# Kernel optimization log

Hardware: AMD Instinct MI355X
Metric: run time of the kernel (lower is better)

The kernel has to match this reference:

```python
import jax, jax.numpy as jnp
import numpy as np

IN_CH = 8        # input_channels (includes time channel)
HID = 64         # hidden_channels
OUT = 1          # output_channels
MLP_W = 128      # CDEFunc hidden width
B, T = 4096, 166


def setup_inputs() -> dict:
    key = jax.random.key(0)
    ks = jax.random.split(key, 12)
    s = lambda fan_in: 1.0 / np.sqrt(fan_in)
    u0 = jax.random.normal(ks[0], (B, IN_CH - 1), dtype=jnp.float32)
    coeffs = jax.random.normal(ks[1], (B, T, IN_CH), dtype=jnp.float32)
    # CDEFunc params
    W1 = jax.random.uniform(ks[2], (HID, MLP_W), jnp.float32, -s(HID), s(HID))
    b1 = jax.random.uniform(ks[3], (MLP_W,), jnp.float32, -s(HID), s(HID))
    W2 = jax.random.uniform(ks[4], (MLP_W, IN_CH * HID), jnp.float32, -s(MLP_W), s(MLP_W))
    b2 = jax.random.uniform(ks[5], (IN_CH * HID,), jnp.float32, -s(MLP_W), s(MLP_W))
    # initial / readout linears
    Wi = jax.random.uniform(ks[6], (IN_CH - 1, HID), jnp.float32, -s(IN_CH - 1), s(IN_CH - 1))
    bi = jax.random.uniform(ks[7], (HID,), jnp.float32, -s(IN_CH - 1), s(IN_CH - 1))
    Wr = jax.random.uniform(ks[8], (HID, OUT), jnp.float32, -s(HID), s(HID))
    br = jax.random.uniform(ks[9], (OUT,), jnp.float32, -s(HID), s(HID))
    return {"u0": u0, "coeffs": coeffs, "W1": W1, "b1": b1, "W2": W2,
            "b2": b2, "Wi": Wi, "bi": bi, "Wr": Wr, "br": br}


def _cde_forward(u0, coeffs, W1, b1, W2, b2, Wi, bi, Wr, br):
    z0 = u0 @ Wi + bi                                  # [B, HID]
    # Linear interpolation on the knot grid t=0..T-1 with Euler steps of dt=1:
    # z_{k+1} = z_k + f(z_k) @ (X_{k+1} - X_k)
    dX = coeffs[:, 1:] - coeffs[:, :-1]                # [B, T-1, IN_CH]
    dX_t = jnp.swapaxes(dX, 0, 1)                      # [T-1, B, IN_CH]

    def step(z, dx):
        h = jax.nn.relu(z @ W1 + b1)                   # [B, MLP_W]
        f = jnp.tanh(h @ W2 + b2)                      # [B, IN_CH*HID]
        f = f.reshape(z.shape[0], HID, IN_CH)          # [B, HID, IN_CH]
        z_new = z + jnp.einsum('bhi,bi->bh', f, dx)
        return z_new, z_new

    _, zs = jax.lax.scan(step, z0, dX_t)               # [T-1, B, HID]
    z_all = jnp.concatenate([z0[None], zs], axis=0)    # [T, B, HID]
    z_all = jnp.swapaxes(z_all, 0, 1)                  # [B, T, HID]
    return z_all @ Wr + br                             # [B, T, OUT]


def reference(u0, coeffs, W1, b1, W2, b2, Wi, bi, Wr, br):
    return _cde_forward(u0, coeffs, W1, b1, W2, b2, Wi, bi, Wr, br)
```

## Files before the change

### kernel.cpp

```cpp
#include <hip/hip_runtime.h>


#define NBLK 256
#define NT   512
#define RB   16
#define T_LEN 166
#define NSTEP 165
#define IC   8
#define HID  64
#define MW   128
#define NF   512

typedef _Float16 half8 __attribute__((ext_vector_type(8)));
typedef _Float16 half4 __attribute__((ext_vector_type(4)));
typedef float    f32x4 __attribute__((ext_vector_type(4)));

__device__ __forceinline__ float fast_tanh(float x) {
    float e = __expf(2.0f * x);
    return 1.0f - 2.0f * __builtin_amdgcn_rcpf(e + 1.0f);
}

__device__ __forceinline__ void bar_lgkm() {
    asm volatile("s_waitcnt lgkmcnt(0)" ::: "memory");
    __builtin_amdgcn_s_barrier();
    __builtin_amdgcn_sched_barrier(0);
}

__device__ __forceinline__ float sum_xor16(float x) {
#if __has_builtin(__builtin_amdgcn_permlane16_swap)
    auto r = __builtin_amdgcn_permlane16_swap(__float_as_uint(x), __float_as_uint(x), false, false);
    return __uint_as_float(r[0]) + __uint_as_float(r[1]);
#else
    return x + __shfl_xor(x, 16, 64);
#endif
}
__device__ __forceinline__ float sum_xor32(float x) {
#if __has_builtin(__builtin_amdgcn_permlane32_swap)
    auto r = __builtin_amdgcn_permlane32_swap(__float_as_uint(x), __float_as_uint(x), false, false);
    return __uint_as_float(r[0]) + __uint_as_float(r[1]);
#else
    return x + __shfl_xor(x, 32, 64);
#endif
}

__global__ __launch_bounds__(NT, 2)
void cde_fused(const float* __restrict__ u0, const float* __restrict__ coeffs,
               const float* __restrict__ W1, const float* __restrict__ b1,
               const float* __restrict__ W2, const float* __restrict__ b2,
               const float* __restrict__ Wi, const float* __restrict__ bi,
               const float* __restrict__ Wr, const float* __restrict__ br,
               float* __restrict__ out)
{
    __shared__ __align__(16) unsigned char hh[RB * 256];
    __shared__ __align__(16) unsigned char hl[RB * 256];
    __shared__ __align__(16) unsigned char zh[RB * 128];
    __shared__ __align__(16) unsigned char zl[RB * 128];
    __shared__ float part[8][17];

    const int tid  = threadIdx.x;
    const int lane = tid & 63;
    const int w    = tid >> 6;
    const int l15  = lane & 15;
    const int lq   = lane >> 4;
    const bool hi32 = (lane & 32) != 0;
    const int swzr = (l15 & 7) << 4;
    const int b0   = blockIdx.x * RB;

    half8 w1h[2], w1l[2];
    #pragma unroll
    for (int kt = 0; kt < 2; ++kt) {
        const int krow = kt * 32 + lq * 8;
        const int ncol = w * 16 + l15;
        half8 vh, vl;
        #pragma unroll
        for (int j = 0; j < 8; ++j) {
            const float x = W1[(krow + j) * MW + ncol];
            const _Float16 hi = (_Float16)x;
            vh[j] = hi; vl[j] = (_Float16)(x - (float)hi);
        }
        w1h[kt] = vh; w1l[kt] = vl;
    }
    half8 w2h[16], w2l[16];
    #pragma unroll
    for (int q = 0; q < 4; ++q) {
        #pragma unroll
        for (int kt = 0; kt < 4; ++kt) {
            const int krow = kt * 32 + lq * 8;
            const int ncol = (w * 4 + q) * 16 + l15;
            half8 vh, vl;
            #pragma unroll
            for (int j = 0; j < 8; ++j) {
                const float x = W2[(krow + j) * NF + ncol];
                const _Float16 hi = (_Float16)x;
                vh[j] = hi; vl[j] = (_Float16)(x - (float)hi);
            }
            w2h[q * 4 + kt] = vh; w2l[q * 4 + kt] = vl;
        }
    }
    const f32x4 b1v = *(const f32x4*)(b1 + w * 16 + lq * 4);
    f32x4 b2v[4];
    #pragma unroll
    for (int q = 0; q < 4; ++q)
        b2v[q] = *(const f32x4*)(b2 + (w * 4 + q) * 16 + lq * 4);

    float wrs[8];
    #pragma unroll
    for (int j = 0; j < 8; ++j) wrs[j] = Wr[w * 8 + j];
    const float brv = br[0];

    float z8[8];
    {
        float uu[7];
        const float* ur = u0 + (size_t)(b0 + l15) * 7;
        #pragma unroll
        for (int c = 0; c < 7; ++c) uu[c] = ur[c];
        #pragma unroll
        for (int j = 0; j < 8; ++j) {
            float a = bi[w * 8 + j];
            #pragma unroll
            for (int c = 0; c < 7; ++c) a = fmaf(uu[c], Wi[c * HID + w * 8 + j], a);
            z8[j] = a;
        }
    }
    {
        half8 hi8, lo8;
        float rp = 0.f;
        #pragma unroll
        for (int j = 0; j < 8; ++j) {
            const _Float16 hi = (_Float16)z8[j];
            hi8[j] = hi; lo8[j] = (_Float16)(z8[j] - (float)hi);
            rp = fmaf(z8[j], wrs[j], rp);
        }
        if (lq == 0) {
            const int zoff = l15 * 128 + ((w * 16) ^ swzr);
            *(half8*)(zh + zoff) = hi8;
            *(half8*)(zl + zoff) = lo8;
            part[w][l15] = rp;
        }
    }
    const float* cbase = coeffs + (size_t)(b0 + l15) * T_LEN * IC + (lq & 1) * 4;
    f32x4 ccur = *(const f32x4*)(cbase);
    __syncthreads();

    for (int t = 0; t < NSTEP; ++t) {
        const f32x4 cnext = *(const f32x4*)(cbase + (size_t)(t + 1) * IC);

        if (w == 7) {
            float v = part[lq][l15] + part[lq + 4][l15];
            v = sum_xor32(sum_xor16(v));
            if (lq == 0) out[(size_t)(b0 + l15) * T_LEN + t] = v + brv;
        }

        const int zo0 = l15 * 128 + ((lq * 16) ^ swzr);
        const int zo1 = l15 * 128 + ((64 + lq * 16) ^ swzr);
        const half8 zfh0 = *(const half8*)(zh + zo0);
        const half8 zfl0 = *(const half8*)(zl + zo0);
        const half8 zfh1 = *(const half8*)(zh + zo1);
        const half8 zfl1 = *(const half8*)(zl + zo1);
        f32x4 a1A = b1v;
        f32x4 a1B = {0.f, 0.f, 0.f, 0.f};
        a1A = __builtin_amdgcn_mfma_f32_16x16x32_f16(w1h[0], zfh0, a1A, 0, 0, 0);
        a1B = __builtin_amdgcn_mfma_f32_16x16x32_f16(w1h[1], zfh1, a1B, 0, 0, 0);
        a1A = __builtin_amdgcn_mfma_f32_16x16x32_f16(w1l[0], zfh0, a1A, 0, 0, 0);
        a1B = __builtin_amdgcn_mfma_f32_16x16x32_f16(w1l[1], zfh1, a1B, 0, 0, 0);
        a1A = __builtin_amdgcn_mfma_f32_16x16x32_f16(w1h[0], zfl0, a1A, 0, 0, 0);
        a1B = __builtin_amdgcn_mfma_f32_16x16x32_f16(w1h[1], zfl1, a1B, 0, 0, 0);
        half4 ph, pl;
        #pragma unroll
        for (int r = 0; r < 4; ++r) {
            const float hv = fmaxf(a1A[r] + a1B[r], 0.0f);
            const _Float16 hi = (_Float16)hv;
            ph[r] = hi; pl[r] = (_Float16)(hv - (float)hi);
        }
        const int hoff = l15 * 256 + ((w * 32 + lq * 8) ^ swzr);
        *(half4*)(hh + hoff) = ph;
        *(half4*)(hl + hoff) = pl;
        bar_lgkm();

        half8 bhf[4], blf[4];
        #pragma unroll
        for (int kt = 0; kt < 4; ++kt) {
            const int off = l15 * 256 + ((kt * 64 + lq * 16) ^ swzr);
            bhf[kt] = *(const half8*)(hh + off);
            blf[kt] = *(const half8*)(hl + off);
        }
        const f32x4 dxv = cnext - ccur;
        float rp = 0.f;
        #pragma unroll
        for (int q = 0; q < 4; ++q) {
            f32x4 acc = b2v[q];
            #pragma unroll
            for (int kt = 0; kt < 4; ++kt) {
                acc = __builtin_amdgcn_mfma_f32_16x16x32_f16(w2h[q * 4 + kt], bhf[kt], acc, 0, 0, 0);
                acc = __builtin_amdgcn_mfma_f32_16x16x32_f16(w2l[q * 4 + kt], bhf[kt], acc, 0, 0, 0);
                acc = __builtin_amdgcn_mfma_f32_16x16x32_f16(w2h[q * 4 + kt], blf[kt], acc, 0, 0, 0);
            }
            float s = 0.f;
            #pragma unroll
            for (int r = 0; r < 4; ++r)
                s = fmaf(fast_tanh(acc[r]), dxv[r], s);
            const float tt = sum_xor16(s);
            const float uu = sum_xor32(hi32 ? tt : 0.f);
            z8[2 * q]     += tt;
            z8[2 * q + 1] += uu;
            rp = fmaf(z8[2 * q], wrs[2 * q], rp);
            rp = fmaf(z8[2 * q + 1], wrs[2 * q + 1], rp);
        }
        {
            half8 hi8, lo8;
            #pragma unroll
            for (int j = 0; j < 8; ++j) {
                const _Float16 hi = (_Float16)z8[j];
                hi8[j] = hi; lo8[j] = (_Float16)(z8[j] - (float)hi);
            }
            if (lq == 0) {
                const int zoff = l15 * 128 + ((w * 16) ^ swzr);
                *(half8*)(zh + zoff) = hi8;
                *(half8*)(zl + zoff) = lo8;
                part[w][l15] = rp;
            }
        }
        ccur = cnext;
        bar_lgkm();
    }

    if (w == 7) {
        float v = part[lq][l15] + part[lq + 4][l15];
        v = sum_xor32(sum_xor16(v));
        if (lq == 0) out[(size_t)(b0 + l15) * T_LEN + NSTEP] = v + brv;
    }
}

extern "C" void kernel_launch(void* const* d_in, const int* in_sizes, int n_in,
                              void* d_out, int out_size, void* d_ws, size_t ws_size,
                              hipStream_t stream) {
    const float* u0     = (const float*)d_in[0];
    const float* coeffs = (const float*)d_in[1];
    const float* W1     = (const float*)d_in[2];
    const float* b1     = (const float*)d_in[3];
    const float* W2     = (const float*)d_in[4];
    const float* b2     = (const float*)d_in[5];
    const float* Wi     = (const float*)d_in[6];
    const float* bi     = (const float*)d_in[7];
    const float* Wr     = (const float*)d_in[8];
    const float* br     = (const float*)d_in[9];
    cde_fused<<<NBLK, NT, 0, stream>>>(u0, coeffs, W1, b1, W2, b2, Wi, bi, Wr, br,
                                       (float*)d_out);
}
```

Measured before the change: 290.0 us.

## Double threads per block, split W2 work across sixteen waves, stage W1 in LDS

Raises the block size from 8 to 16 waves so each wave handles two W2 column tiles instead of four, halving per-wave serial MFMA and tanh work on the recurrent critical path. W1 fragments move from registers into shared memory, and only the first eight waves run the first layer. Each wave now owns 4 hidden units instead of 8, and the readout reduction sums 16 partials. The risks are higher barrier cost with more waves, idle waves during the W1 phase, and register pressure under the tighter launch bounds.

```diff
diff --git a/kernel.cpp b/kernel.cpp
--- a/kernel.cpp
+++ b/kernel.cpp
@@ -2,7 +2,7 @@
 
 
 #define NBLK 256
-#define NT   512
+#define NT   1024
 #define RB   16
 #define T_LEN 166
 #define NSTEP 165
@@ -43,7 +43,7 @@
 #endif
 }
 
-__global__ __launch_bounds__(NT, 2)
+__global__ __launch_bounds__(NT, 4)
 void cde_fused(const float* __restrict__ u0, const float* __restrict__ coeffs,
                const float* __restrict__ W1, const float* __restrict__ b1,
                const float* __restrict__ W2, const float* __restrict__ b2,
@@ -55,7 +55,8 @@
     __shared__ __align__(16) unsigned char hl[RB * 256];
     __shared__ __align__(16) unsigned char zh[RB * 128];
     __shared__ __align__(16) unsigned char zl[RB * 128];
-    __shared__ float part[8][17];
+    __shared__ __align__(16) unsigned char w1f[8 * 64 * 80];
+    __shared__ float part[16][17];
 
     const int tid  = threadIdx.x;
     const int lane = tid & 63;
@@ -66,27 +67,13 @@
     const int swzr = (l15 & 7) << 4;
     const int b0   = blockIdx.x * RB;
 
-    half8 w1h[2], w1l[2];
+    half8 w2h[8], w2l[8];
     #pragma unroll
-    for (int kt = 0; kt < 2; ++kt) {
-        const int krow = kt * 32 + lq * 8;
-        const int ncol = w * 16 + l15;
-        half8 vh, vl;
-        #pragma unroll
-        for (int j = 0; j < 8; ++j) {
-            const float x = W1[(krow + j) * MW + ncol];
-            const _Float16 hi = (_Float16)x;
-            vh[j] = hi; vl[j] = (_Float16)(x - (float)hi);
-        }
-        w1h[kt] = vh; w1l[kt] = vl;
-    }
-    half8 w2h[16], w2l[16];
-    #pragma unroll
-    for (int q = 0; q < 4; ++q) {
+    for (int q = 0; q < 2; ++q) {
         #pragma unroll
         for (int kt = 0; kt < 4; ++kt) {
             const int krow = kt * 32 + lq * 8;
-            const int ncol = (w * 4 + q) * 16 + l15;
+            const int ncol = (w * 2 + q) * 16 + l15;
             half8 vh, vl;
             #pragma unroll
             for (int j = 0; j < 8; ++j) {
@@ -97,44 +84,64 @@
             w2h[q * 4 + kt] = vh; w2l[q * 4 + kt] = vl;
         }
     }
-    const f32x4 b1v = *(const f32x4*)(b1 + w * 16 + lq * 4);
-    f32x4 b2v[4];
+    f32x4 b2v[2];
     #pragma unroll
-    for (int q = 0; q < 4; ++q)
-        b2v[q] = *(const f32x4*)(b2 + (w * 4 + q) * 16 + lq * 4);
-
-    float wrs[8];
+    for (int q = 0; q < 2; ++q)
+        b2v[q] = *(const f32x4*)(b2 + (w * 2 + q) * 16 + lq * 4);
+
+    f32x4 b1v = {0.f, 0.f, 0.f, 0.f};
+    const int fbase = (w * 64 + lane) * 80;
+    if (w < 8) {
+        #pragma unroll
+        for (int kt = 0; kt < 2; ++kt) {
+            const int krow = kt * 32 + lq * 8;
+            const int ncol = w * 16 + l15;
+            half8 vh, vl;
+            #pragma unroll
+            for (int j = 0; j < 8; ++j) {
+                const float x = W1[(krow + j) * MW + ncol];
+                const _Float16 hi = (_Float16)x;
+                vh[j] = hi; vl[j] = (_Float16)(x - (float)hi);
+            }
+            *(half8*)(w1f + fbase + kt * 16)      = vh;
+            *(half8*)(w1f + fbase + 32 + kt * 16) = vl;
+        }
+        b1v = *(const f32x4*)(b1 + w * 16 + lq * 4);
+    }
+
+    const int w_u = __builtin_amdgcn_readfirstlane(w);
+    float wrs[4];
     #pragma unroll
-    for (int j = 0; j < 8; ++j) wrs[j] = Wr[w * 8 + j];
+    for (int j = 0; j < 4; ++j) wrs[j] = Wr[w_u * 4 + j];
     const float brv = br[0];
 
-    float z8[8];
+    float z4[4];
     {
-        float uu[7];
+        float uu7[7];
         const float* ur = u0 + (size_t)(b0 + l15) * 7;
         #pragma unroll
-        for (int c = 0; c < 7; ++c) uu[c] = ur[c];
-        #pragma unroll
-        for (int j = 0; j < 8; ++j) {
-            float a = bi[w * 8 + j];
-            #pragma unroll
-            for (int c = 0; c < 7; ++c) a = fmaf(uu[c], Wi[c * HID + w * 8 + j], a);
-            z8[j] = a;
+        for (int c = 0; c < 7; ++c) uu7[c] = ur[c];
+        #pragma unroll
+        for (int j = 0; j < 4; ++j) {
+            float a = bi[w * 4 + j];
+            #pragma unroll
+            for (int c = 0; c < 7; ++c) a = fmaf(uu7[c], Wi[c * HID + w * 4 + j], a);
+            z4[j] = a;
         }
     }
     {
-        half8 hi8, lo8;
+        half4 h4, l4;
         float rp = 0.f;
         #pragma unroll
-        for (int j = 0; j < 8; ++j) {
-            const _Float16 hi = (_Float16)z8[j];
-            hi8[j] = hi; lo8[j] = (_Float16)(z8[j] - (float)hi);
-            rp = fmaf(z8[j], wrs[j], rp);
+        for (int j = 0; j < 4; ++j) {
+            const _Float16 hi = (_Float16)z4[j];
+            h4[j] = hi; l4[j] = (_Float16)(z4[j] - (float)hi);
+            rp = fmaf(z4[j], wrs[j], rp);
         }
         if (lq == 0) {
-            const int zoff = l15 * 128 + ((w * 16) ^ swzr);
-            *(half8*)(zh + zoff) = hi8;
-            *(half8*)(zl + zoff) = lo8;
+            const int zoff = l15 * 128 + ((w * 8) ^ swzr);
+            *(half4*)(zh + zoff) = h4;
+            *(half4*)(zl + zoff) = l4;
             part[w][l15] = rp;
         }
     }
@@ -145,78 +152,87 @@
     for (int t = 0; t < NSTEP; ++t) {
         const f32x4 cnext = *(const f32x4*)(cbase + (size_t)(t + 1) * IC);
 
-        if (w == 7) {
-            float v = part[lq][l15] + part[lq + 4][l15];
+        if (w == 15) {
+            float v = part[lq * 4 + 0][l15] + part[lq * 4 + 1][l15]
+                    + part[lq * 4 + 2][l15] + part[lq * 4 + 3][l15];
             v = sum_xor32(sum_xor16(v));
             if (lq == 0) out[(size_t)(b0 + l15) * T_LEN + t] = v + brv;
         }
 
-        const int zo0 = l15 * 128 + ((lq * 16) ^ swzr);
-        const int zo1 = l15 * 128 + ((64 + lq * 16) ^ swzr);
-        const half8 zfh0 = *(const half8*)(zh + zo0);
-        const half8 zfl0 = *(const half8*)(zl + zo0);
-        const half8 zfh1 = *(const half8*)(zh + zo1);
-        const half8 zfl1 = *(const half8*)(zl + zo1);
-        f32x4 a1A = b1v;
-        f32x4 a1B = {0.f, 0.f, 0.f, 0.f};
-        a1A = __builtin_amdgcn_mfma_f32_16x16x32_f16(w1h[0], zfh0, a1A, 0, 0, 0);
-        a1B = __builtin_amdgcn_mfma_f32_16x16x32_f16(w1h[1], zfh1, a1B, 0, 0, 0);
-        a1A = __builtin_amdgcn_mfma_f32_16x16x32_f16(w1l[0], zfh0, a1A, 0, 0, 0);
-        a1B = __builtin_amdgcn_mfma_f32_16x16x32_f16(w1l[1], zfh1, a1B, 0, 0, 0);
-        a1A = __builtin_amdgcn_mfma_f32_16x16x32_f16(w1h[0], zfl0, a1A, 0, 0, 0);
-        a1B = __builtin_amdgcn_mfma_f32_16x16x32_f16(w1h[1], zfl1, a1B, 0, 0, 0);
-        half4 ph, pl;
-        #pragma unroll
-        for (int r = 0; r < 4; ++r) {
-            const float hv = fmaxf(a1A[r] + a1B[r], 0.0f);
-            const _Float16 hi = (_Float16)hv;
-            ph[r] = hi; pl[r] = (_Float16)(hv - (float)hi);
-        }
-        const int hoff = l15 * 256 + ((w * 32 + lq * 8) ^ swzr);
-        *(half4*)(hh + hoff) = ph;
-        *(half4*)(hl + hoff) = pl;
+        if (w < 8) {
+            const int zo0 = l15 * 128 + ((lq * 16) ^ swzr);
+            const int zo1 = l15 * 128 + ((64 + lq * 16) ^ swzr);
+            half8 fh = *(const half8*)(w1f + fbase);
+            half8 fl = *(const half8*)(w1f + fbase + 32);
+            const half8 zfh0 = *(const half8*)(zh + zo0);
+            const half8 zfl0 = *(const half8*)(zl + zo0);
+            f32x4 a1A = b1v;
+            a1A = __builtin_amdgcn_mfma_f32_16x16x32_f16(fh, zfh0, a1A, 0, 0, 0);
+            a1A = __builtin_amdgcn_mfma_f32_16x16x32_f16(fl, zfh0, a1A, 0, 0, 0);
+            a1A = __builtin_amdgcn_mfma_f32_16x16x32_f16(fh, zfl0, a1A, 0, 0, 0);
+            fh = *(const half8*)(w1f + fbase + 16);
+            fl = *(const half8*)(w1f + fbase + 48);
+            const half8 zfh1 = *(const half8*)(zh + zo1);
+            const half8 zfl1 = *(const half8*)(zl + zo1);
+            a1A = __builtin_amdgcn_mfma_f32_16x16x32_f16(fh, zfh1, a1A, 0, 0, 0);
+            a1A = __builtin_amdgcn_mfma_f32_16x16x32_f16(fl, zfh1, a1A, 0, 0, 0);
+            a1A = __builtin_amdgcn_mfma_f32_16x16x32_f16(fh, zfl1, a1A, 0, 0, 0);
+            half4 ph, pl;
+            #pragma unroll
+            for (int r = 0; r < 4; ++r) {
+                const float hv = fmaxf(a1A[r], 0.0f);
+                const _Float16 hi = (_Float16)hv;
+                ph[r] = hi; pl[r] = (_Float16)(hv - (float)hi);
+            }
+            const int hoff = l15 * 256 + ((w * 32 + lq * 8) ^ swzr);
+            *(half4*)(hh + hoff) = ph;
+            *(half4*)(hl + hoff) = pl;
+        }
         bar_lgkm();
 
-        half8 bhf[4], blf[4];
+        f32x4 acc0 = b2v[0];
+        f32x4 acc1 = b2v[1];
         #pragma unroll
         for (int kt = 0; kt < 4; ++kt) {
             const int off = l15 * 256 + ((kt * 64 + lq * 16) ^ swzr);
-            bhf[kt] = *(const half8*)(hh + off);
-            blf[kt] = *(const half8*)(hl + off);
-        }
+            const half8 bh = *(const half8*)(hh + off);
+            const half8 bl = *(const half8*)(hl + off);
+            acc0 = __builtin_amdgcn_mfma_f32_16x16x32_f16(w2h[kt],     bh, acc0, 0, 0, 0);
+            acc1 = __builtin_amdgcn_mfma_f32_16x16x32_f16(w2h[4 + kt], bh, acc1, 0, 0, 0);
+            acc0 = __builtin_amdgcn_mfma_f32_16x16x32_f16(w2l[kt],     bh, acc0, 0, 0, 0);
+            acc1 = __builtin_amdgcn_mfma_f32_16x16x32_f16(w2l[4 + kt], bh, acc1, 0, 0, 0);
+            acc0 = __builtin_amdgcn_mfma_f32_16x16x32_f16(w2h[kt],     bl, acc0, 0, 0, 0);
+            acc1 = __builtin_amdgcn_mfma_f32_16x16x32_f16(w2h[4 + kt], bl, acc1, 0, 0, 0);
+        }
+
         const f32x4 dxv = cnext - ccur;
-        float rp = 0.f;
-        #pragma unroll
-        for (int q = 0; q < 4; ++q) {
-            f32x4 acc = b2v[q];
-            #pragma unroll
-            for (int kt = 0; kt < 4; ++kt) {
-                acc = __builtin_amdgcn_mfma_f32_16x16x32_f16(w2h[q * 4 + kt], bhf[kt], acc, 0, 0, 0);
-                acc = __builtin_amdgcn_mfma_f32_16x16x32_f16(w2l[q * 4 + kt], bhf[kt], acc, 0, 0, 0);
-                acc = __builtin_amdgcn_mfma_f32_16x16x32_f16(w2h[q * 4 + kt], blf[kt], acc, 0, 0, 0);
-            }
-            float s = 0.f;
-            #pragma unroll
-            for (int r = 0; r < 4; ++r)
-                s = fmaf(fast_tanh(acc[r]), dxv[r], s);
-            const float tt = sum_xor16(s);
-            const float uu = sum_xor32(hi32 ? tt : 0.f);
-            z8[2 * q]     += tt;
-            z8[2 * q + 1] += uu;
-            rp = fmaf(z8[2 * q], wrs[2 * q], rp);
-            rp = fmaf(z8[2 * q + 1], wrs[2 * q + 1], rp);
+        float s0 = 0.f, s1 = 0.f;
+        #pragma unroll
+        for (int r = 0; r < 4; ++r) {
+            s0 = fmaf(fast_tanh(acc0[r]), dxv[r], s0);
+            s1 = fmaf(fast_tanh(acc1[r]), dxv[r], s1);
         }
         {
-            half8 hi8, lo8;
-            #pragma unroll
-            for (int j = 0; j < 8; ++j) {
-                const _Float16 hi = (_Float16)z8[j];
-                hi8[j] = hi; lo8[j] = (_Float16)(z8[j] - (float)hi);
+            const float tt0 = sum_xor16(s0);
+            const float uu0 = sum_xor32(hi32 ? tt0 : 0.f);
+            z4[0] += tt0; z4[1] += uu0;
+            const float tt1 = sum_xor16(s1);
+            const float uu1 = sum_xor32(hi32 ? tt1 : 0.f);
+            z4[2] += tt1; z4[3] += uu1;
+        }
+        {
+            half4 h4, l4;
+            float rp = 0.f;
+            #pragma unroll
+            for (int j = 0; j < 4; ++j) {
+                const _Float16 hi = (_Float16)z4[j];
+                h4[j] = hi; l4[j] = (_Float16)(z4[j] - (float)hi);
+                rp = fmaf(z4[j], wrs[j], rp);
             }
             if (lq == 0) {
-                const int zoff = l15 * 128 + ((w * 16) ^ swzr);
-                *(half8*)(zh + zoff) = hi8;
-                *(half8*)(zl + zoff) = lo8;
+                const int zoff = l15 * 128 + ((w * 8) ^ swzr);
+                *(half4*)(zh + zoff) = h4;
+                *(half4*)(zl + zoff) = l4;
                 part[w][l15] = rp;
             }
         }
@@ -224,8 +240,9 @@
         bar_lgkm();
     }
 
-    if (w == 7) {
-        float v = part[lq][l15] + part[lq + 4][l15];
+    if (w == 15) {
+        float v = part[lq * 4 + 0][l15] + part[lq * 4 + 1][l15]
+                + part[lq * 4 + 2][l15] + part[lq * 4 + 3][l15];
         v = sum_xor32(sum_xor16(v));
         if (lq == 0) out[(size_t)(b0 + l15) * T_LEN + NSTEP] = v + brv;
     }
```

New measurement: 289.4 us. No clear change (-0.2%).
